# Kernel optimization log

Measured on AMD Instinct MI355X. Metric: run time of the kernel, lower is better.

The kernel has to match this reference:

```python
import jax, jax.numpy as jnp
import numpy as np

B, T, C, H = 2, 2048, 1024, 16
D = C // H  # head_dim = 64
CH = C // 2


def _ln(x, g, b, eps=1e-5):
    m = x.mean(-1, keepdims=True)
    v = ((x - m) ** 2).mean(-1, keepdims=True)
    return (x - m) / jnp.sqrt(v + eps) * g + b


def setup_inputs() -> dict:
    key = jax.random.key(0)
    ks = iter(jax.random.split(key, 32))
    w = lambda shp: jax.random.normal(next(ks), shp, dtype=jnp.float32) * 0.02
    inp = {
        'x': jax.random.normal(next(ks), (B, T, C), dtype=jnp.float32),
        'attention_mask': jnp.ones((B, T, T), dtype=jnp.int32),
        # importance_net: Linear(C,C/2), LN(C/2), GELU, Linear(C/2,1), Sigmoid
        'imp_w1': w((C, CH)), 'imp_b1': jnp.zeros((CH,)),
        'imp_g': jnp.ones((CH,)), 'imp_beta': jnp.zeros((CH,)),
        'imp_w2': w((CH, 1)), 'imp_b2': jnp.zeros((1,)),
        # reasoning_net: Linear(C,C), LN(C), GELU, Linear(C,C)
        'rsn_w1': w((C, C)), 'rsn_b1': jnp.zeros((C,)),
        'rsn_g': jnp.ones((C,)), 'rsn_beta': jnp.zeros((C,)),
        'rsn_w2': w((C, C)), 'rsn_b2': jnp.zeros((C,)),
        # attention projections
        'q_w': w((C, C)), 'q_b': jnp.zeros((C,)),
        'k_w': w((C, C)), 'k_b': jnp.zeros((C,)),
        'v_w': w((C, C)), 'v_b': jnp.zeros((C,)),
        'o_w': w((C, C)), 'o_b': jnp.zeros((C,)),
        # temp_net: Linear(C,C/2), LN(C/2), GELU, Linear(C/2,H)
        'tmp_w1': w((C, CH)), 'tmp_b1': jnp.zeros((CH,)),
        'tmp_g': jnp.ones((CH,)), 'tmp_beta': jnp.zeros((CH,)),
        'tmp_w2': w((CH, H)), 'tmp_b2': jnp.zeros((H,)),
        # output LayerNorm
        'norm_g': jnp.ones((C,)), 'norm_b': jnp.zeros((C,)),
    }
    return inp


def reference(x, attention_mask, imp_w1, imp_b1, imp_g, imp_beta, imp_w2, imp_b2,
              rsn_w1, rsn_b1, rsn_g, rsn_beta, rsn_w2, rsn_b2,
              q_w, q_b, k_w, k_b, v_w, v_b, o_w, o_b,
              tmp_w1, tmp_b1, tmp_g, tmp_beta, tmp_w2, tmp_b2,
              norm_g, norm_b):
    Bz, Tz, Cz = x.shape
    # importance gating: [B,T,1]
    h = jax.nn.gelu(_ln(x @ imp_w1 + imp_b1, imp_g, imp_beta), approximate=False)
    importance = jnp.maximum(jax.nn.sigmoid(h @ imp_w2 + imp_b2), 1e-6)
    xi = x * importance
    # reasoning net on gated input
    h = jax.nn.gelu(_ln(xi @ rsn_w1 + rsn_b1, rsn_g, rsn_beta), approximate=False)
    reasoned = h @ rsn_w2 + rsn_b2
    # projections
    q = (reasoned @ q_w + q_b).reshape(Bz, Tz, H, D).transpose(0, 2, 1, 3)
    k = (xi @ k_w + k_b).reshape(Bz, Tz, H, D).transpose(0, 2, 1, 3)
    v = (x @ v_w + v_b).reshape(Bz, Tz, H, D).transpose(0, 2, 1, 3)
    # per-(batch,head) temperature
    ht = jax.nn.gelu(_ln(reasoned.mean(axis=1) @ tmp_w1 + tmp_b1, tmp_g, tmp_beta), approximate=False)
    temp = jax.nn.softplus(ht @ tmp_w2 + tmp_b2) + 0.5  # [B,H]
    # attention with mask and learned temperature before softmax
    scale = 1.0 / jnp.sqrt(jnp.float32(D))
    attn = jnp.einsum('bhqd,bhkd->bhqk', q, k) * scale
    attn = jnp.where(attention_mask[:, None] == 0, -jnp.inf, attn)
    attn = attn * temp[:, :, None, None]
    attn = jax.nn.softmax(attn, axis=-1)
    # dropout is identity in eval mode
    out = jnp.einsum('bhqk,bhkd->bhqd', attn, v)
    out = out.transpose(0, 2, 1, 3).reshape(Bz, Tz, Cz)
    out = out @ o_w + o_b
    return _ln(x + out, norm_g, norm_b)
```

## Files before the change

### kernel.cpp

```cpp
#include <hip/hip_runtime.h>
#include <hip/hip_bf16.h>
#include <math.h>

#define BB 2
#define TT 2048
#define CC 1024
#define HH 16
#define DD 64
#define CHALF 512
#define NN (BB * TT)
#define LOG2E 1.44269504088896340736f

typedef __attribute__((ext_vector_type(8))) short short8;
typedef __attribute__((ext_vector_type(4))) short short4_t;
typedef __attribute__((ext_vector_type(4))) float f32x4;

__device__ __forceinline__ float gelu_exact(float x) {
    return 0.5f * x * (1.0f + erff(x * 0.70710678118654752f));
}

__device__ __forceinline__ short f2bf(float f) {
    __hip_bfloat16 h = __float2bfloat16(f);
    short s;
    __builtin_memcpy(&s, &h, 2);
    return s;
}

__device__ __forceinline__ float bf2f(short s) {
    __hip_bfloat16 h;
    __builtin_memcpy(&h, &s, 2);
    return __bfloat162float(h);
}

__device__ __forceinline__ short4_t pack_bf16x4(float a, float b, float c,
                                                float d) {
    short4_t s4;
    s4[0] = f2bf(a);
    s4[1] = f2bf(b);
    s4[2] = f2bf(c);
    s4[3] = f2bf(d);
    return s4;
}

__device__ __forceinline__ void async_copy16(const void* g, void* l) {
    __builtin_amdgcn_global_load_lds(
        (const __attribute__((address_space(1))) void*)g,
        (__attribute__((address_space(3))) void*)l, 16, 0, 0);
}

__global__ __launch_bounds__(256) void prep(
    const float* __restrict__ x, __hip_bfloat16* __restrict__ x_bf,
    const int* __restrict__ mask, int* __restrict__ flags,
    const float* w0, const float* w1, const float* w2, const float* w3,
    const float* w4, const float* w5, const float* w6,
    __hip_bfloat16* t0, __hip_bfloat16* t1, __hip_bfloat16* t2,
    __hip_bfloat16* t3, __hip_bfloat16* t4, __hip_bfloat16* t5,
    __hip_bfloat16* t6) {
    __shared__ float T[64][65];
    int blk = blockIdx.x;
    int tid = threadIdx.x;
    if (blk < 2048) {
        int i = (blk * 256 + tid) * 8;
        float4 a = *(const float4*)&x[i];
        float4 b = *(const float4*)&x[i + 4];
        __hip_bfloat16 o[8] = {
            __float2bfloat16(a.x), __float2bfloat16(a.y),
            __float2bfloat16(a.z), __float2bfloat16(a.w),
            __float2bfloat16(b.x), __float2bfloat16(b.y),
            __float2bfloat16(b.z), __float2bfloat16(b.w)};
        *(float4*)&x_bf[i] = *(float4*)o;
    } else if (blk < 4096) {
        int idx = blk - 2048;
        int kt = idx & 31, qt = (idx >> 5) & 31, b = idx >> 10;
        int* red = (int*)T;
        int r = tid >> 2;
        int c0 = (tid & 3) * 16;
        const int* base =
            mask + ((size_t)(b * TT + qt * 64 + r)) * TT + kt * 64 + c0;
        int all = 1;
#pragma unroll
        for (int i = 0; i < 4; ++i) {
            int4 m4 = *(const int4*)(base + i * 4);
            all &= (m4.x != 0) & (m4.y != 0) & (m4.z != 0) & (m4.w != 0);
        }
        red[tid] = all;
        __syncthreads();
#pragma unroll
        for (int o = 128; o > 0; o >>= 1) {
            if (tid < o) red[tid] &= red[tid + o];
            __syncthreads();
        }
        if (tid == 0) flags[(b * 32 + qt) * 32 + kt] = red[0];
    } else {
        int idx = blk - 4096;
        const float* W;
        __hip_bfloat16* Wt;
        int N, n0, k0;
        if (idx < 128) {
            W = w0; Wt = t0; N = 512;
            n0 = (idx & 7) * 64;
            k0 = (idx >> 3) * 64;
        } else {
            idx -= 128;
            int w = idx >> 8;
            int r = idx & 255;
            N = 1024;
            n0 = (r & 15) * 64;
            k0 = (r >> 4) * 64;
            switch (w) {
                case 0: W = w1; Wt = t1; break;
                case 1: W = w2; Wt = t2; break;
                case 2: W = w3; Wt = t3; break;
                case 3: W = w4; Wt = t4; break;
                case 4: W = w5; Wt = t5; break;
                default: W = w6; Wt = t6; break;
            }
        }
        int c = tid & 63, r4 = tid >> 6;
#pragma unroll
        for (int i = 0; i < 16; ++i) {
            int row = i * 4 + r4;
            T[row][c] = W[(size_t)(k0 + row) * N + n0 + c];
        }
        __syncthreads();
#pragma unroll
        for (int i = 0; i < 16; ++i) {
            int row = i * 4 + r4;
            Wt[(size_t)(n0 + row) * CC + k0 + c] = __float2bfloat16(T[c][row]);
        }
    }
}

template <bool BF16OUT>
__global__ __launch_bounds__(256) void gemm_mfma64(
    const short* __restrict__ A, const short* __restrict__ Wt,
    const float* __restrict__ bias, float* __restrict__ Cf,
    __hip_bfloat16* __restrict__ Cb, int M, int N, int K) {
    __shared__ short As0[64][32], As1[64][32];
    __shared__ short Bs0[128][32], Bs1[128][32];
    int tid = threadIdx.x;
    int wave = tid >> 6, lane = tid & 63;
    int m16 = lane & 15, quad = lane >> 4;
    int wm = wave >> 1, wn = wave & 1;
    int row0 = blockIdx.y * 64, col0 = blockIdx.x * 128;
    int lr = lane >> 2;
    int kof = (lane & 3) * 8;

    f32x4 acc[2][4];
#pragma unroll
    for (int i = 0; i < 2; ++i)
#pragma unroll
        for (int j = 0; j < 4; ++j) acc[i][j] = (f32x4){0.f, 0.f, 0.f, 0.f};

    for (int k0 = 0; k0 < K; k0 += 64) {
        const short* arow = A + (size_t)(row0 + wave * 16 + lr) * K + k0 + kof;
        async_copy16(arow, &As0[wave * 16][0]);
        async_copy16(arow + 32, &As1[wave * 16][0]);
#pragma unroll
        for (int j = 0; j < 2; ++j) {
            int rbase = wave * 32 + j * 16;
            const short* brow =
                Wt + (size_t)(col0 + rbase + lr) * K + k0 + kof;
            async_copy16(brow, &Bs0[rbase][0]);
            async_copy16(brow + 32, &Bs1[rbase][0]);
        }
        __syncthreads();
#pragma unroll
        for (int kc = 0; kc < 2; ++kc) {
            short8 af[2], bfr[4];
#pragma unroll
            for (int i = 0; i < 2; ++i)
                af[i] = kc ? *(const short8*)&As1[wm * 32 + i * 16 + m16][quad * 8]
                           : *(const short8*)&As0[wm * 32 + i * 16 + m16][quad * 8];
#pragma unroll
            for (int j = 0; j < 4; ++j)
                bfr[j] = kc ? *(const short8*)&Bs1[wn * 64 + j * 16 + m16][quad * 8]
                            : *(const short8*)&Bs0[wn * 64 + j * 16 + m16][quad * 8];
#pragma unroll
            for (int i = 0; i < 2; ++i)
#pragma unroll
                for (int j = 0; j < 4; ++j)
                    acc[i][j] = __builtin_amdgcn_mfma_f32_16x16x32_bf16(
                        af[i], bfr[j], acc[i][j], 0, 0, 0);
        }
        __syncthreads();
    }
#pragma unroll
    for (int i = 0; i < 2; ++i) {
#pragma unroll
        for (int j = 0; j < 4; ++j) {
            int col = col0 + wn * 64 + j * 16 + m16;
            float bv = bias[col];
#pragma unroll
            for (int rr = 0; rr < 4; ++rr) {
                int row = row0 + wm * 32 + i * 16 + quad * 4 + rr;
                float val = acc[i][j][rr] + bv;
                if (BF16OUT)
                    Cb[(size_t)row * N + col] = __float2bfloat16(val);
                else
                    Cf[(size_t)row * N + col] = val;
            }
        }
    }
}

__global__ __launch_bounds__(256) void gemm_qkv(
    const short* __restrict__ Aq, const short* __restrict__ Ak,
    const short* __restrict__ Av, const short* __restrict__ Wq,
    const short* __restrict__ Wk, const short* __restrict__ Wv,
    const float* __restrict__ bq, const float* __restrict__ bk,
    const float* __restrict__ bv, __hip_bfloat16* __restrict__ Cq,
    __hip_bfloat16* __restrict__ Ck, __hip_bfloat16* __restrict__ Cv,
    const float* __restrict__ tmp) {
    int z = blockIdx.z;
    const short* A = (z == 0) ? Aq : (z == 1) ? Ak : Av;
    const short* Wt = (z == 0) ? Wq : (z == 1) ? Wk : Wv;
    const float* bias = (z == 0) ? bq : (z == 1) ? bk : bv;

    __shared__ short As0[128][32], As1[128][32];
    __shared__ short Bs0[128][32], Bs1[128][32];
    int tid = threadIdx.x;
    int wave = tid >> 6, lane = tid & 63;
    int m16 = lane & 15, quad = lane >> 4;
    int wm = wave >> 1, wn = wave & 1;
    int row0 = blockIdx.y * 128, col0 = blockIdx.x * 128;
    int lr = lane >> 2;
    int kof = (lane & 3) * 8;

    float scale = 1.0f;
    if (z == 0)
        scale = tmp[(row0 >> 11) * HH + (col0 >> 6) + wn] * 0.125f * LOG2E;

    f32x4 acc[4][4];
#pragma unroll
    for (int i = 0; i < 4; ++i)
#pragma unroll
        for (int j = 0; j < 4; ++j) acc[i][j] = (f32x4){0.f, 0.f, 0.f, 0.f};

    for (int k0 = 0; k0 < CC; k0 += 64) {
#pragma unroll
        for (int j = 0; j < 2; ++j) {
            int rbase = wave * 32 + j * 16;
            const short* ar = A + (size_t)(row0 + rbase + lr) * CC + k0 + kof;
            async_copy16(ar, &As0[rbase][0]);
            async_copy16(ar + 32, &As1[rbase][0]);
            const short* br = Wt + (size_t)(col0 + rbase + lr) * CC + k0 + kof;
            async_copy16(br, &Bs0[rbase][0]);
            async_copy16(br + 32, &Bs1[rbase][0]);
        }
        __syncthreads();
#pragma unroll
        for (int kc = 0; kc < 2; ++kc) {
            short8 af[4], bfr[4];
#pragma unroll
            for (int i = 0; i < 4; ++i)
                af[i] = kc ? *(const short8*)&As1[wm * 64 + i * 16 + m16][quad * 8]
                           : *(const short8*)&As0[wm * 64 + i * 16 + m16][quad * 8];
#pragma unroll
            for (int j = 0; j < 4; ++j)
                bfr[j] = kc ? *(const short8*)&Bs1[wn * 64 + j * 16 + m16][quad * 8]
                            : *(const short8*)&Bs0[wn * 64 + j * 16 + m16][quad * 8];
#pragma unroll
            for (int i = 0; i < 4; ++i)
#pragma unroll
                for (int j = 0; j < 4; ++j)
                    acc[i][j] = __builtin_amdgcn_mfma_f32_16x16x32_bf16(
                        af[i], bfr[j], acc[i][j], 0, 0, 0);
        }
        __syncthreads();
    }
    if (z == 2) {
        int b = row0 >> 11;
        int t0r = (row0 & (TT - 1)) + wm * 64 + quad * 4;
#pragma unroll
        for (int i = 0; i < 4; ++i) {
#pragma unroll
            for (int j = 0; j < 4; ++j) {
                int col = col0 + wn * 64 + j * 16 + m16;
                int h = col >> 6, d = col & 63;
                float bv2 = bias[col];
                short4_t pk = pack_bf16x4(
                    acc[i][j][0] + bv2, acc[i][j][1] + bv2,
                    acc[i][j][2] + bv2, acc[i][j][3] + bv2);
                *(short4_t*)&Cv[(((size_t)(b * HH + h) * DD) + d) * TT + t0r +
                                i * 16] = pk;
            }
        }
    } else {
        __hip_bfloat16* C = (z == 0) ? Cq : Ck;
#pragma unroll
        for (int i = 0; i < 4; ++i) {
#pragma unroll
            for (int j = 0; j < 4; ++j) {
                int col = col0 + wn * 64 + j * 16 + m16;
                float bv2 = bias[col];
#pragma unroll
                for (int rr = 0; rr < 4; ++rr) {
                    int row = row0 + wm * 64 + i * 16 + quad * 4 + rr;
                    C[(size_t)row * CC + col] =
                        __float2bfloat16((acc[i][j][rr] + bv2) * scale);
                }
            }
        }
    }
}

__global__ __launch_bounds__(256) void imp_fused(
    const float* __restrict__ h1, const float* __restrict__ g,
    const float* __restrict__ beta, const float* __restrict__ w2,
    const float* __restrict__ b2, const float* __restrict__ x,
    __hip_bfloat16* __restrict__ xi) {
    int row = blockIdx.x;
    int tid = threadIdx.x;
    const float* hr = h1 + (size_t)row * CHALF;
    float v0 = hr[tid], v1 = hr[tid + 256];
    __shared__ float red[256];
    red[tid] = v0 + v1;
    __syncthreads();
#pragma unroll
    for (int o = 128; o > 0; o >>= 1) {
        if (tid < o) red[tid] += red[tid + o];
        __syncthreads();
    }
    float mean = red[0] * (1.0f / CHALF);
    __syncthreads();
    float d0 = v0 - mean, d1 = v1 - mean;
    red[tid] = d0 * d0 + d1 * d1;
    __syncthreads();
#pragma unroll
    for (int o = 128; o > 0; o >>= 1) {
        if (tid < o) red[tid] += red[tid + o];
        __syncthreads();
    }
    float inv = rsqrtf(red[0] * (1.0f / CHALF) + 1e-5f);
    __syncthreads();
    float ge0 = gelu_exact(d0 * inv * g[tid] + beta[tid]);
    float ge1 = gelu_exact(d1 * inv * g[tid + 256] + beta[tid + 256]);
    red[tid] = ge0 * w2[tid] + ge1 * w2[tid + 256];
    __syncthreads();
#pragma unroll
    for (int o = 128; o > 0; o >>= 1) {
        if (tid < o) red[tid] += red[tid + o];
        __syncthreads();
    }
    float z = red[0] + b2[0];
    float sg = 1.0f / (1.0f + expf(-z));
    float imp = fmaxf(sg, 1e-6f);
#pragma unroll
    for (int i = 0; i < 4; ++i) {
        int c = i * 256 + tid;
        xi[(size_t)row * CC + c] =
            __float2bfloat16(x[(size_t)row * CC + c] * imp);
    }
}

__global__ __launch_bounds__(256) void ln_gelu_bb(
    const __hip_bfloat16* __restrict__ Y, const float* __restrict__ g,
    const float* __restrict__ beta, __hip_bfloat16* __restrict__ O) {
    int row = blockIdx.x;
    int tid = threadIdx.x;
    int c0 = tid * 4;
    short4_t raw = *(const short4_t*)&Y[(size_t)row * CC + c0];
    float v[4];
    float s = 0.f;
#pragma unroll
    for (int i = 0; i < 4; ++i) {
        v[i] = bf2f(raw[i]);
        s += v[i];
    }
    __shared__ float red[256];
    red[tid] = s;
    __syncthreads();
#pragma unroll
    for (int o = 128; o > 0; o >>= 1) {
        if (tid < o) red[tid] += red[tid + o];
        __syncthreads();
    }
    float mean = red[0] * (1.0f / CC);
    __syncthreads();
    s = 0.f;
#pragma unroll
    for (int i = 0; i < 4; ++i) {
        float d = v[i] - mean;
        s += d * d;
    }
    red[tid] = s;
    __syncthreads();
#pragma unroll
    for (int o = 128; o > 0; o >>= 1) {
        if (tid < o) red[tid] += red[tid + o];
        __syncthreads();
    }
    float inv = rsqrtf(red[0] * (1.0f / CC) + 1e-5f);
    float4 gg = *(const float4*)&g[c0];
    float4 bb = *(const float4*)&beta[c0];
    short4_t ov = pack_bf16x4(
        gelu_exact((v[0] - mean) * inv * gg.x + bb.x),
        gelu_exact((v[1] - mean) * inv * gg.y + bb.y),
        gelu_exact((v[2] - mean) * inv * gg.z + bb.z),
        gelu_exact((v[3] - mean) * inv * gg.w + bb.w));
    *(short4_t*)&O[(size_t)row * CC + c0] = ov;
}

__global__ __launch_bounds__(256) void mean_part(
    const __hip_bfloat16* __restrict__ R, float* __restrict__ part) {
    int idx = blockIdx.x * 256 + threadIdx.x;
    int c = idx & (CC - 1);
    int chunk = (idx >> 10) & 15;
    int b = idx >> 14;
    const __hip_bfloat16* base = R + ((size_t)(b * TT + chunk * 128)) * CC + c;
    float s = 0.f;
    for (int t = 0; t < 128; ++t) s += __bfloat162float(base[(size_t)t * CC]);
    part[idx] = s;
}

__global__ __launch_bounds__(256) void temp_gemv1(
    const float* __restrict__ part, const float* __restrict__ w1,
    const float* __restrict__ b1, float* __restrict__ acc1) {
    __shared__ float rm_l[CC];
    __shared__ float red[256];
    int b = blockIdx.y;
    int c0 = blockIdx.x * 64;
    int tid = threadIdx.x;
    for (int cc = tid; cc < CC; cc += 256) {
        float s = 0.f;
#pragma unroll
        for (int ch = 0; ch < 16; ++ch)
            s += part[(size_t)(b * 16 + ch) * CC + cc];
        rm_l[cc] = s * (1.0f / TT);
    }
    __syncthreads();
    int col = c0 + (tid & 63);
    int kq = tid >> 6;
    float s = 0.f;
#pragma unroll 8
    for (int i = kq * 256; i < kq * 256 + 256; ++i)
        s = fmaf(rm_l[i], w1[(size_t)i * CHALF + col], s);
    red[tid] = s;
    __syncthreads();
    if (tid < 64) {
        float t = red[tid] + red[tid + 64] + red[tid + 128] + red[tid + 192];
        acc1[b * CHALF + tid + c0] = t + b1[col];
    }
}

__global__ __launch_bounds__(512) void temp_fin(
    const float* __restrict__ acc1, const float* __restrict__ g,
    const float* __restrict__ beta, const float* __restrict__ w2,
    const float* __restrict__ b2, float* __restrict__ temp) {
    __shared__ float red[512];
    __shared__ float wred[8][16];
    int b = blockIdx.x;
    int tid = threadIdx.x;
    int wave = tid >> 6, lane = tid & 63;
    float acc = acc1[b * CHALF + tid];
    red[tid] = acc;
    __syncthreads();
#pragma unroll
    for (int o = 256; o > 0; o >>= 1) {
        if (tid < o) red[tid] += red[tid + o];
        __syncthreads();
    }
    float mean = red[0] * (1.0f / CHALF);
    __syncthreads();
    float d = acc - mean;
    red[tid] = d * d;
    __syncthreads();
#pragma unroll
    for (int o = 256; o > 0; o >>= 1) {
        if (tid < o) red[tid] += red[tid + o];
        __syncthreads();
    }
    float inv = rsqrtf(red[0] * (1.0f / CHALF) + 1e-5f);
    float ht = gelu_exact((acc - mean) * inv * g[tid] + beta[tid]);
    float p[16];
#pragma unroll
    for (int j = 0; j < 16; ++j) p[j] = ht * w2[tid * HH + j];
#pragma unroll
    for (int off = 1; off < 64; off <<= 1)
#pragma unroll
        for (int j = 0; j < 16; ++j) p[j] += __shfl_xor(p[j], off, 64);
    if (lane == 0)
#pragma unroll
        for (int j = 0; j < 16; ++j) wred[wave][j] = p[j];
    __syncthreads();
    if (tid < HH) {
        float s = b2[tid];
#pragma unroll
        for (int w = 0; w < 8; ++w) s += wred[w][tid];
        float sp = fmaxf(s, 0.f) + log1pf(expf(-fabsf(s)));
        temp[b * HH + tid] = sp + 0.5f;
    }
}

__global__ __launch_bounds__(256) void flash_attn_mfma(
    const short* __restrict__ q, const short* __restrict__ k,
    const short* __restrict__ vt, const int* __restrict__ mask,
    const int* __restrict__ flags, __hip_bfloat16* __restrict__ out) {
    __shared__ short Ks[64][72];
    __shared__ short Vt[64][72];
    __shared__ short Ps[128][72];
    int tid = threadIdx.x;
    int wave = tid >> 6, lane = tid & 63;
    int m16 = lane & 15, quad = lane >> 4;
    int qt = blockIdx.x;
    int q0 = qt * 128;
    int bh = blockIdx.y;
    int b = bh >> 4, h = bh & 15;

    short8 qf[2][2];
#pragma unroll
    for (int qg = 0; qg < 2; ++qg) {
        const short* qrow = q + ((size_t)(b * TT + q0 + wave * 32 + qg * 16 + m16)) * CC +
                            h * DD + quad * 8;
        qf[qg][0] = *(const short8*)(qrow);
        qf[qg][1] = *(const short8*)(qrow + 32);
    }

    float m_run[2] = {-INFINITY, -INFINITY};
    float l_run[2] = {0.f, 0.f};
    f32x4 acc_o[2][4];
#pragma unroll
    for (int qg = 0; qg < 2; ++qg)
#pragma unroll
        for (int t = 0; t < 4; ++t) acc_o[qg][t] = (f32x4){0.f, 0.f, 0.f, 0.f};

    for (int kt = 0; kt < TT / 64; ++kt) {
        int kb = kt * 64;
#pragma unroll
        for (int i = 0; i < 2; ++i) {
            int idx = i * 256 + tid;
            int r = idx >> 3;
            int dc = (idx & 7) * 8;
            *(short8*)&Ks[r][dc] =
                *(const short8*)(k + ((size_t)(b * TT + kb + r)) * CC + h * DD + dc);
            *(short8*)&Vt[r][dc] =
                *(const short8*)(vt + ((size_t)bh * DD + r) * TT + kb + dc);
        }
        __syncthreads();

        short8 kf[4][2];
#pragma unroll
        for (int t = 0; t < 4; ++t) {
            kf[t][0] = *(const short8*)&Ks[t * 16 + m16][quad * 8];
            kf[t][1] = *(const short8*)&Ks[t * 16 + m16][32 + quad * 8];
        }
        int fl = flags[(b * 32 + 2 * qt + (wave >> 1)) * 32 + kt];

#pragma unroll
        for (int qg = 0; qg < 2; ++qg) {
            f32x4 sacc[4];
#pragma unroll
            for (int t = 0; t < 4; ++t) sacc[t] = (f32x4){0.f, 0.f, 0.f, 0.f};
#pragma unroll
            for (int t = 0; t < 4; ++t) {
                sacc[t] = __builtin_amdgcn_mfma_f32_16x16x32_bf16(kf[t][0], qf[qg][0], sacc[t], 0, 0, 0);
                sacc[t] = __builtin_amdgcn_mfma_f32_16x16x32_bf16(kf[t][1], qf[qg][1], sacc[t], 0, 0, 0);
            }
            float sv[4][4];
#pragma unroll
            for (int t = 0; t < 4; ++t)
#pragma unroll
                for (int r = 0; r < 4; ++r) sv[t][r] = sacc[t][r];
            if (fl == 0) {
                int qrow = q0 + wave * 32 + qg * 16 + m16;
#pragma unroll
                for (int t = 0; t < 4; ++t)
#pragma unroll
                    for (int r = 0; r < 4; ++r) {
                        int kg = kb + t * 16 + quad * 4 + r;
                        if (mask[((size_t)(b * TT + qrow)) * TT + kg] == 0)
                            sv[t][r] = -INFINITY;
                    }
            }
            float mx = sv[0][0];
#pragma unroll
            for (int t = 0; t < 4; ++t)
#pragma unroll
                for (int r = 0; r < 4; ++r) mx = fmaxf(mx, sv[t][r]);
            mx = fmaxf(mx, __shfl_xor(mx, 16, 64));
            mx = fmaxf(mx, __shfl_xor(mx, 32, 64));
            float mnew = fmaxf(m_run[qg], mx);
            if (__any(mnew > m_run[qg])) {
                float alpha = __builtin_amdgcn_exp2f(m_run[qg] - mnew);
                l_run[qg] *= alpha;
#pragma unroll
                for (int td = 0; td < 4; ++td)
#pragma unroll
                    for (int r = 0; r < 4; ++r) acc_o[qg][td][r] *= alpha;
            }
            m_run[qg] = mnew;
            int prow = wave * 32 + qg * 16 + m16;
            float psum = 0.f;
#pragma unroll
            for (int t = 0; t < 4; ++t) {
                short4_t pk;
#pragma unroll
                for (int r = 0; r < 4; ++r) {
                    float p = __builtin_amdgcn_exp2f(sv[t][r] - mnew);
                    psum += p;
                    pk[r] = f2bf(p);
                }
                *(short4_t*)&Ps[prow][t * 16 + quad * 4] = pk;
            }
            psum += __shfl_xor(psum, 16, 64);
            psum += __shfl_xor(psum, 32, 64);
            l_run[qg] += psum;
        }

#pragma unroll
        for (int kc = 0; kc < 2; ++kc) {
            short8 vf[4];
#pragma unroll
            for (int td = 0; td < 4; ++td)
                vf[td] = *(const short8*)&Vt[td * 16 + m16][kc * 32 + quad * 8];
#pragma unroll
            for (int qg = 0; qg < 2; ++qg) {
                short8 pf = *(const short8*)&Ps[wave * 32 + qg * 16 + m16][kc * 32 + quad * 8];
#pragma unroll
                for (int td = 0; td < 4; ++td)
                    acc_o[qg][td] = __builtin_amdgcn_mfma_f32_16x16x32_bf16(
                        vf[td], pf, acc_o[qg][td], 0, 0, 0);
            }
        }
        __syncthreads();
    }

#pragma unroll
    for (int qg = 0; qg < 2; ++qg) {
        float inv = 1.0f / l_run[qg];
        int row = b * TT + q0 + wave * 32 + qg * 16 + m16;
#pragma unroll
        for (int td = 0; td < 4; ++td) {
            short4_t pk = pack_bf16x4(
                acc_o[qg][td][0] * inv, acc_o[qg][td][1] * inv,
                acc_o[qg][td][2] * inv, acc_o[qg][td][3] * inv);
            *(short4_t*)&out[(size_t)row * CC + h * DD + td * 16 + quad * 4] = pk;
        }
    }
}

__global__ __launch_bounds__(256) void final_ln_b(
    const float* __restrict__ x, const __hip_bfloat16* __restrict__ p,
    const float* __restrict__ g, const float* __restrict__ beta,
    float* __restrict__ out) {
    int row = blockIdx.x;
    int tid = threadIdx.x;
    int c0 = tid * 4;
    float4 xv = *(const float4*)&x[(size_t)row * CC + c0];
    short4_t pv = *(const short4_t*)&p[(size_t)row * CC + c0];
    float v[4] = {xv.x + bf2f(pv[0]), xv.y + bf2f(pv[1]),
                  xv.z + bf2f(pv[2]), xv.w + bf2f(pv[3])};
    float s = v[0] + v[1] + v[2] + v[3];
    __shared__ float red[256];
    red[tid] = s;
    __syncthreads();
#pragma unroll
    for (int o = 128; o > 0; o >>= 1) {
        if (tid < o) red[tid] += red[tid + o];
        __syncthreads();
    }
    float mean = red[0] * (1.0f / CC);
    __syncthreads();
    s = 0.f;
#pragma unroll
    for (int i = 0; i < 4; ++i) {
        float d = v[i] - mean;
        s += d * d;
    }
    red[tid] = s;
    __syncthreads();
#pragma unroll
    for (int o = 128; o > 0; o >>= 1) {
        if (tid < o) red[tid] += red[tid + o];
        __syncthreads();
    }
    float inv = rsqrtf(red[0] * (1.0f / CC) + 1e-5f);
    float4 gg = *(const float4*)&g[c0];
    float4 bb = *(const float4*)&beta[c0];
    float4 ov = {(v[0] - mean) * inv * gg.x + bb.x,
                 (v[1] - mean) * inv * gg.y + bb.y,
                 (v[2] - mean) * inv * gg.z + bb.z,
                 (v[3] - mean) * inv * gg.w + bb.w};
    *(float4*)&out[(size_t)row * CC + c0] = ov;
}

extern "C" void kernel_launch(void* const* d_in, const int* in_sizes, int n_in,
                              void* d_out, int out_size, void* d_ws,
                              size_t ws_size, hipStream_t stream) {
    const float* x        = (const float*)d_in[0];
    const int*   mask     = (const int*)d_in[1];
    const float* imp_w1   = (const float*)d_in[2];
    const float* imp_b1   = (const float*)d_in[3];
    const float* imp_g    = (const float*)d_in[4];
    const float* imp_beta = (const float*)d_in[5];
    const float* imp_w2   = (const float*)d_in[6];
    const float* imp_b2   = (const float*)d_in[7];
    const float* rsn_w1   = (const float*)d_in[8];
    const float* rsn_b1   = (const float*)d_in[9];
    const float* rsn_g    = (const float*)d_in[10];
    const float* rsn_beta = (const float*)d_in[11];
    const float* rsn_w2   = (const float*)d_in[12];
    const float* rsn_b2   = (const float*)d_in[13];
    const float* q_w      = (const float*)d_in[14];
    const float* q_b      = (const float*)d_in[15];
    const float* k_w      = (const float*)d_in[16];
    const float* k_b      = (const float*)d_in[17];
    const float* v_w      = (const float*)d_in[18];
    const float* v_b      = (const float*)d_in[19];
    const float* o_w      = (const float*)d_in[20];
    const float* o_b      = (const float*)d_in[21];
    const float* tmp_w1   = (const float*)d_in[22];
    const float* tmp_b1   = (const float*)d_in[23];
    const float* tmp_g    = (const float*)d_in[24];
    const float* tmp_beta = (const float*)d_in[25];
    const float* tmp_w2   = (const float*)d_in[26];
    const float* tmp_b2   = (const float*)d_in[27];
    const float* norm_g   = (const float*)d_in[28];
    const float* norm_b   = (const float*)d_in[29];
    float* out = (float*)d_out;
    float* ws  = (float*)d_ws;

    float* h1  = ws;
    __hip_bfloat16* g1b   = (__hip_bfloat16*)(ws + 2097152);
    __hip_bfloat16* x_bf  = (__hip_bfloat16*)(ws + 6291456);
    __hip_bfloat16* xi_bf = (__hip_bfloat16*)(ws + 8388608);
    __hip_bfloat16* h2b   = (__hip_bfloat16*)(ws + 10485760);
    __hip_bfloat16* rs_bf = (__hip_bfloat16*)(ws + 12582912);
    __hip_bfloat16* qb    = (__hip_bfloat16*)(ws + 14680064);
    __hip_bfloat16* kb    = (__hip_bfloat16*)(ws + 16777216);
    __hip_bfloat16* vtb   = (__hip_bfloat16*)(ws + 20971520);
    __hip_bfloat16* imp_w1t = (__hip_bfloat16*)(ws + 23068672);
    __hip_bfloat16* rsn_w1t = (__hip_bfloat16*)(ws + 23330816);
    __hip_bfloat16* rsn_w2t = (__hip_bfloat16*)(ws + 23855104);
    __hip_bfloat16* q_wt    = (__hip_bfloat16*)(ws + 24379392);
    __hip_bfloat16* k_wt    = (__hip_bfloat16*)(ws + 24903680);
    __hip_bfloat16* v_wt    = (__hip_bfloat16*)(ws + 25427968);
    __hip_bfloat16* o_wt    = (__hip_bfloat16*)(ws + 25952256);
    float* tmp  = ws + 26478592;
    float* part = ws + 26479104;
    int*   flg  = (int*)(ws + 26511872);
    float* acc1 = ws + 26513920;

    dim3 blk(256);
    prep<<<5760, blk, 0, stream>>>(
        x, x_bf, mask, flg,
        imp_w1, rsn_w1, rsn_w2, q_w, k_w, v_w, o_w,
        imp_w1t, rsn_w1t, rsn_w2t, q_wt, k_wt, v_wt, o_wt);

    gemm_mfma64<false><<<dim3(CHALF / 128, NN / 64), blk, 0, stream>>>(
        (const short*)x_bf, (const short*)imp_w1t, imp_b1, h1, nullptr, NN, CHALF, CC);
    imp_fused<<<NN, blk, 0, stream>>>(h1, imp_g, imp_beta, imp_w2, imp_b2, x, xi_bf);
    gemm_mfma64<true><<<dim3(CC / 128, NN / 64), blk, 0, stream>>>(
        (const short*)xi_bf, (const short*)rsn_w1t, rsn_b1, nullptr, g1b, NN, CC, CC);
    ln_gelu_bb<<<NN, blk, 0, stream>>>(g1b, rsn_g, rsn_beta, h2b);
    gemm_mfma64<true><<<dim3(CC / 128, NN / 64), blk, 0, stream>>>(
        (const short*)h2b, (const short*)rsn_w2t, rsn_b2, nullptr, rs_bf, NN, CC, CC);
    mean_part<<<128, blk, 0, stream>>>(rs_bf, part);
    temp_gemv1<<<dim3(CHALF / 64, BB), blk, 0, stream>>>(part, tmp_w1, tmp_b1, acc1);
    temp_fin<<<BB, dim3(512), 0, stream>>>(acc1, tmp_g, tmp_beta, tmp_w2, tmp_b2, tmp);
    gemm_qkv<<<dim3(CC / 128, NN / 128, 3), blk, 0, stream>>>(
        (const short*)rs_bf, (const short*)xi_bf, (const short*)x_bf,
        (const short*)q_wt, (const short*)k_wt, (const short*)v_wt,
        q_b, k_b, v_b, qb, kb, vtb, tmp);
    flash_attn_mfma<<<dim3(TT / 128, BB * HH), blk, 0, stream>>>(
        (const short*)qb, (const short*)kb, (const short*)vtb, mask, flg, rs_bf);
    gemm_mfma64<true><<<dim3(CC / 128, NN / 64), blk, 0, stream>>>(
        (const short*)rs_bf, (const short*)o_wt, o_b, nullptr, g1b, NN, CC, CC);
    final_ln_b<<<NN, blk, 0, stream>>>(x, g1b, norm_g, norm_b, out);
}
```

Baseline: 412.7 us.

## Split flash attention over the key dimension and merge the halves in a combine kernel

```diff
diff --git a/kernel.cpp b/kernel.cpp
--- a/kernel.cpp
+++ b/kernel.cpp
@@ -496,7 +496,8 @@
 __global__ __launch_bounds__(256) void flash_attn_mfma(
     const short* __restrict__ q, const short* __restrict__ k,
     const short* __restrict__ vt, const int* __restrict__ mask,
-    const int* __restrict__ flags, __hip_bfloat16* __restrict__ out) {
+    const int* __restrict__ flags, __hip_bfloat16* __restrict__ po,
+    float* __restrict__ ml) {
     __shared__ short Ks[64][72];
     __shared__ short Vt[64][72];
     __shared__ short Ps[128][72];
@@ -507,6 +508,7 @@
     int q0 = qt * 128;
     int bh = blockIdx.y;
     int b = bh >> 4, h = bh & 15;
+    int zi = blockIdx.z;
 
     short8 qf[2][2];
 #pragma unroll
@@ -525,7 +527,7 @@
 #pragma unroll
         for (int t = 0; t < 4; ++t) acc_o[qg][t] = (f32x4){0.f, 0.f, 0.f, 0.f};
 
-    for (int kt = 0; kt < TT / 64; ++kt) {
+    for (int kt = zi * 16; kt < zi * 16 + 16; ++kt) {
         int kb = kt * 64;
 #pragma unroll
         for (int i = 0; i < 2; ++i) {
@@ -628,16 +630,42 @@
 
 #pragma unroll
     for (int qg = 0; qg < 2; ++qg) {
-        float inv = 1.0f / l_run[qg];
-        int row = b * TT + q0 + wave * 32 + qg * 16 + m16;
+        int qrow = q0 + wave * 32 + qg * 16 + m16;
+        size_t base = ((size_t)zi * (BB * HH) + bh) * TT + qrow;
+        if (quad == 0) {
+            float2 v2 = make_float2(m_run[qg], l_run[qg]);
+            *(float2*)&ml[base * 2] = v2;
+        }
 #pragma unroll
         for (int td = 0; td < 4; ++td) {
-            short4_t pk = pack_bf16x4(
-                acc_o[qg][td][0] * inv, acc_o[qg][td][1] * inv,
-                acc_o[qg][td][2] * inv, acc_o[qg][td][3] * inv);
-            *(short4_t*)&out[(size_t)row * CC + h * DD + td * 16 + quad * 4] = pk;
-        }
-    }
+            short4_t pk = pack_bf16x4(acc_o[qg][td][0], acc_o[qg][td][1],
+                                      acc_o[qg][td][2], acc_o[qg][td][3]);
+            *(short4_t*)&po[base * DD + td * 16 + quad * 4] = pk;
+        }
+    }
+}
+
+__global__ __launch_bounds__(256) void flash_combine(
+    const __hip_bfloat16* __restrict__ po, const float* __restrict__ ml,
+    __hip_bfloat16* __restrict__ out) {
+    int i = blockIdx.x * 256 + threadIdx.x;
+    int d0 = (i & 15) * 4;
+    int qg = i >> 4;
+    float2 ml0 = *(const float2*)&ml[(size_t)qg * 2];
+    float2 ml1 = *(const float2*)&ml[(size_t)(65536 + qg) * 2];
+    float m = fmaxf(ml0.x, ml1.x);
+    float w0 = __builtin_amdgcn_exp2f(ml0.x - m);
+    float w1 = __builtin_amdgcn_exp2f(ml1.x - m);
+    float inv = 1.0f / (ml0.y * w0 + ml1.y * w1);
+    short4_t o0 = *(const short4_t*)&po[(size_t)qg * DD + d0];
+    short4_t o1 = *(const short4_t*)&po[(size_t)(65536 + qg) * DD + d0];
+    int bh = qg >> 11, qrow = qg & (TT - 1);
+    int b = bh >> 4, h = bh & 15;
+    short4_t ov;
+#pragma unroll
+    for (int r = 0; r < 4; ++r)
+        ov[r] = f2bf((bf2f(o0[r]) * w0 + bf2f(o1[r]) * w1) * inv);
+    *(short4_t*)&out[((size_t)(b * TT + qrow)) * CC + h * DD + d0] = ov;
 }
 
 __global__ __launch_bounds__(256) void final_ln_b(
@@ -723,6 +751,7 @@
 
     float* h1  = ws;
     __hip_bfloat16* g1b   = (__hip_bfloat16*)(ws + 2097152);
+    __hip_bfloat16* po    = (__hip_bfloat16*)ws;
     __hip_bfloat16* x_bf  = (__hip_bfloat16*)(ws + 6291456);
     __hip_bfloat16* xi_bf = (__hip_bfloat16*)(ws + 8388608);
     __hip_bfloat16* h2b   = (__hip_bfloat16*)(ws + 10485760);
@@ -741,6 +770,7 @@
     float* part = ws + 26479104;
     int*   flg  = (int*)(ws + 26511872);
     float* acc1 = ws + 26513920;
+    float* ml   = ws + 26514944;
 
     dim3 blk(256);
     prep<<<5760, blk, 0, stream>>>(
@@ -763,8 +793,10 @@
         (const short*)rs_bf, (const short*)xi_bf, (const short*)x_bf,
         (const short*)q_wt, (const short*)k_wt, (const short*)v_wt,
         q_b, k_b, v_b, qb, kb, vtb, tmp);
-    flash_attn_mfma<<<dim3(TT / 128, BB * HH), blk, 0, stream>>>(
-        (const short*)qb, (const short*)kb, (const short*)vtb, mask, flg, rs_bf);
+    flash_attn_mfma<<<dim3(TT / 128, BB * HH, 2), blk, 0, stream>>>(
+        (const short*)qb, (const short*)kb, (const short*)vtb, mask, flg,
+        po, ml);
+    flash_combine<<<4096, blk, 0, stream>>>(po, ml, rs_bf);
     gemm_mfma64<true><<<dim3(CC / 128, NN / 64), blk, 0, stream>>>(
         (const short*)rs_bf, (const short*)o_wt, o_b, nullptr, g1b, NN, CC, CC);
     final_ln_b<<<NN, blk, 0, stream>>>(x, g1b, norm_g, norm_b, out);
```

After: 423.3 us. 2.6% more time.

## Fold reasoning_net second linear into Q projection weights

Applied to the files above, without the earlier changes.

```diff
diff --git a/kernel.cpp b/kernel.cpp
--- a/kernel.cpp
+++ b/kernel.cpp
@@ -93,9 +93,21 @@
         if (tid == 0) flags[(b * 32 + qt) * 32 + kt] = red[0];
     } else {
         int idx = blk - 4096;
+        if (idx >= 1408) {
+            int i = (idx - 1408) * 2048 + tid * 8;
+            float4 a = *(const float4*)&w2[i];
+            float4 b = *(const float4*)&w2[i + 4];
+            __hip_bfloat16 o[8] = {
+                __float2bfloat16(a.x), __float2bfloat16(a.y),
+                __float2bfloat16(a.z), __float2bfloat16(a.w),
+                __float2bfloat16(b.x), __float2bfloat16(b.y),
+                __float2bfloat16(b.z), __float2bfloat16(b.w)};
+            *(float4*)&t2[i] = *(float4*)o;
+            return;
+        }
         const float* W;
         __hip_bfloat16* Wt;
-        int N, n0, k0;
+        int N = 1024, n0, k0;
         if (idx < 128) {
             W = w0; Wt = t0; N = 512;
             n0 = (idx & 7) * 64;
@@ -104,15 +116,13 @@
             idx -= 128;
             int w = idx >> 8;
             int r = idx & 255;
-            N = 1024;
             n0 = (r & 15) * 64;
             k0 = (r >> 4) * 64;
             switch (w) {
                 case 0: W = w1; Wt = t1; break;
-                case 1: W = w2; Wt = t2; break;
-                case 2: W = w3; Wt = t3; break;
-                case 3: W = w4; Wt = t4; break;
-                case 4: W = w5; Wt = t5; break;
+                case 1: W = w3; Wt = t3; break;
+                case 2: W = w4; Wt = t4; break;
+                case 3: W = w5; Wt = t5; break;
                 default: W = w6; Wt = t6; break;
             }
         }
@@ -305,6 +315,25 @@
     }
 }
 
+__global__ __launch_bounds__(256) void bias_qc_kernel(
+    const short* __restrict__ q_wt, const float* __restrict__ rsn_b2,
+    const float* __restrict__ q_b, float* __restrict__ bias_qc) {
+    int j = blockIdx.x * 4 + (threadIdx.x >> 6);
+    int lane = threadIdx.x & 63;
+    const short* row = q_wt + (size_t)j * CC + lane * 16;
+    short8 a0 = *(const short8*)row;
+    short8 a1 = *(const short8*)(row + 8);
+    float s = 0.f;
+#pragma unroll
+    for (int u = 0; u < 8; ++u) s = fmaf(bf2f(a0[u]), rsn_b2[lane * 16 + u], s);
+#pragma unroll
+    for (int u = 0; u < 8; ++u)
+        s = fmaf(bf2f(a1[u]), rsn_b2[lane * 16 + 8 + u], s);
+#pragma unroll
+    for (int off = 1; off < 64; off <<= 1) s += __shfl_xor(s, off, 64);
+    if (lane == 0) bias_qc[j] = s + q_b[j];
+}
+
 __global__ __launch_bounds__(256) void imp_fused(
     const float* __restrict__ h1, const float* __restrict__ g,
     const float* __restrict__ beta, const float* __restrict__ w2,
@@ -414,21 +443,45 @@
     part[idx] = s;
 }
 
+__global__ __launch_bounds__(256) void rm_proj(
+    const float* __restrict__ part, const short* __restrict__ rsn_w2r,
+    const float* __restrict__ rsn_b2, float* __restrict__ rm) {
+    __shared__ float mh[CC];
+    __shared__ float red[256];
+    int b = blockIdx.y;
+    int c0 = blockIdx.x * 64;
+    int tid = threadIdx.x;
+    for (int cc = tid; cc < CC; cc += 256) {
+        float s = 0.f;
+#pragma unroll
+        for (int ch = 0; ch < 16; ++ch)
+            s += part[(size_t)(b * 16 + ch) * CC + cc];
+        mh[cc] = s * (1.0f / TT);
+    }
+    __syncthreads();
+    int col = c0 + (tid & 63);
+    int kq = tid >> 6;
+    float s = 0.f;
+#pragma unroll 8
+    for (int i = kq * 256; i < kq * 256 + 256; ++i)
+        s = fmaf(mh[i], bf2f(rsn_w2r[(size_t)i * CC + col]), s);
+    red[tid] = s;
+    __syncthreads();
+    if (tid < 64) {
+        float t = red[tid] + red[tid + 64] + red[tid + 128] + red[tid + 192];
+        rm[b * CC + c0 + tid] = t + rsn_b2[c0 + tid];
+    }
+}
+
 __global__ __launch_bounds__(256) void temp_gemv1(
-    const float* __restrict__ part, const float* __restrict__ w1,
+    const float* __restrict__ rm, const float* __restrict__ w1,
     const float* __restrict__ b1, float* __restrict__ acc1) {
     __shared__ float rm_l[CC];
     __shared__ float red[256];
     int b = blockIdx.y;
     int c0 = blockIdx.x * 64;
     int tid = threadIdx.x;
-    for (int cc = tid; cc < CC; cc += 256) {
-        float s = 0.f;
-#pragma unroll
-        for (int ch = 0; ch < 16; ++ch)
-            s += part[(size_t)(b * 16 + ch) * CC + cc];
-        rm_l[cc] = s * (1.0f / TT);
-    }
+    for (int cc = tid; cc < CC; cc += 256) rm_l[cc] = rm[b * CC + cc];
     __syncthreads();
     int col = c0 + (tid & 63);
     int kq = tid >> 6;
@@ -727,12 +780,13 @@
     __hip_bfloat16* xi_bf = (__hip_bfloat16*)(ws + 8388608);
     __hip_bfloat16* h2b   = (__hip_bfloat16*)(ws + 10485760);
     __hip_bfloat16* rs_bf = (__hip_bfloat16*)(ws + 12582912);
+    __hip_bfloat16* w_qct = rs_bf;
     __hip_bfloat16* qb    = (__hip_bfloat16*)(ws + 14680064);
+    __hip_bfloat16* rsn_w2r = qb;
     __hip_bfloat16* kb    = (__hip_bfloat16*)(ws + 16777216);
     __hip_bfloat16* vtb   = (__hip_bfloat16*)(ws + 20971520);
     __hip_bfloat16* imp_w1t = (__hip_bfloat16*)(ws + 23068672);
     __hip_bfloat16* rsn_w1t = (__hip_bfloat16*)(ws + 23330816);
-    __hip_bfloat16* rsn_w2t = (__hip_bfloat16*)(ws + 23855104);
     __hip_bfloat16* q_wt    = (__hip_bfloat16*)(ws + 24379392);
     __hip_bfloat16* k_wt    = (__hip_bfloat16*)(ws + 24903680);
     __hip_bfloat16* v_wt    = (__hip_bfloat16*)(ws + 25427968);
@@ -741,28 +795,36 @@
     float* part = ws + 26479104;
     int*   flg  = (int*)(ws + 26511872);
     float* acc1 = ws + 26513920;
+    float* zeros   = ws + 26514944;
+    float* bias_qc = ws + 26515968;
+    float* rm      = ws + 26516992;
 
     dim3 blk(256);
-    prep<<<5760, blk, 0, stream>>>(
+    hipMemsetAsync(zeros, 0, 1024 * sizeof(float), stream);
+    prep<<<6016, blk, 0, stream>>>(
         x, x_bf, mask, flg,
         imp_w1, rsn_w1, rsn_w2, q_w, k_w, v_w, o_w,
-        imp_w1t, rsn_w1t, rsn_w2t, q_wt, k_wt, v_wt, o_wt);
-
+        imp_w1t, rsn_w1t, rsn_w2r, q_wt, k_wt, v_wt, o_wt);
+    gemm_mfma64<true><<<dim3(CC / 128, 1024 / 64), blk, 0, stream>>>(
+        (const short*)q_wt, (const short*)rsn_w2r, zeros, nullptr, w_qct,
+        1024, CC, CC);
+    bias_qc_kernel<<<256, blk, 0, stream>>>((const short*)q_wt, rsn_b2, q_b,
+                                            bias_qc);
     gemm_mfma64<false><<<dim3(CHALF / 128, NN / 64), blk, 0, stream>>>(
         (const short*)x_bf, (const short*)imp_w1t, imp_b1, h1, nullptr, NN, CHALF, CC);
     imp_fused<<<NN, blk, 0, stream>>>(h1, imp_g, imp_beta, imp_w2, imp_b2, x, xi_bf);
     gemm_mfma64<true><<<dim3(CC / 128, NN / 64), blk, 0, stream>>>(
         (const short*)xi_bf, (const short*)rsn_w1t, rsn_b1, nullptr, g1b, NN, CC, CC);
     ln_gelu_bb<<<NN, blk, 0, stream>>>(g1b, rsn_g, rsn_beta, h2b);
-    gemm_mfma64<true><<<dim3(CC / 128, NN / 64), blk, 0, stream>>>(
-        (const short*)h2b, (const short*)rsn_w2t, rsn_b2, nullptr, rs_bf, NN, CC, CC);
-    mean_part<<<128, blk, 0, stream>>>(rs_bf, part);
-    temp_gemv1<<<dim3(CHALF / 64, BB), blk, 0, stream>>>(part, tmp_w1, tmp_b1, acc1);
+    mean_part<<<128, blk, 0, stream>>>(h2b, part);
+    rm_proj<<<dim3(CC / 64, BB), blk, 0, stream>>>(part, (const short*)rsn_w2r,
+                                                   rsn_b2, rm);
+    temp_gemv1<<<dim3(CHALF / 64, BB), blk, 0, stream>>>(rm, tmp_w1, tmp_b1, acc1);
     temp_fin<<<BB, dim3(512), 0, stream>>>(acc1, tmp_g, tmp_beta, tmp_w2, tmp_b2, tmp);
     gemm_qkv<<<dim3(CC / 128, NN / 128, 3), blk, 0, stream>>>(
-        (const short*)rs_bf, (const short*)xi_bf, (const short*)x_bf,
-        (const short*)q_wt, (const short*)k_wt, (const short*)v_wt,
-        q_b, k_b, v_b, qb, kb, vtb, tmp);
+        (const short*)h2b, (const short*)xi_bf, (const short*)x_bf,
+        (const short*)w_qct, (const short*)k_wt, (const short*)v_wt,
+        bias_qc, k_b, v_b, qb, kb, vtb, tmp);
     flash_attn_mfma<<<dim3(TT / 128, BB * HH), blk, 0, stream>>>(
         (const short*)qb, (const short*)kb, (const short*)vtb, mask, flg, rs_bf);
     gemm_mfma64<true><<<dim3(CC / 128, NN / 64), blk, 0, stream>>>(
```

Result: slower. 438.4 us (+6.2%).

## Double-buffer K/V tiles in flash attention with register prefetch

Applied to the files above, without the earlier changes.

```diff
diff --git a/kernel.cpp b/kernel.cpp
--- a/kernel.cpp
+++ b/kernel.cpp
@@ -497,8 +497,8 @@
     const short* __restrict__ q, const short* __restrict__ k,
     const short* __restrict__ vt, const int* __restrict__ mask,
     const int* __restrict__ flags, __hip_bfloat16* __restrict__ out) {
-    __shared__ short Ks[64][72];
-    __shared__ short Vt[64][72];
+    __shared__ short Ks[2][64][72];
+    __shared__ short Vt[2][64][72];
     __shared__ short Ps[128][72];
     int tid = threadIdx.x;
     int wave = tid >> 6, lane = tid & 63;
@@ -508,6 +508,14 @@
     int bh = blockIdx.y;
     int b = bh >> 4, h = bh & 15;
 
+    int sr[2], sdc[2];
+#pragma unroll
+    for (int i = 0; i < 2; ++i) {
+        int idx = i * 256 + tid;
+        sr[i] = idx >> 3;
+        sdc[i] = (idx & 7) * 8;
+    }
+
     short8 qf[2][2];
 #pragma unroll
     for (int qg = 0; qg < 2; ++qg) {
@@ -525,25 +533,36 @@
 #pragma unroll
         for (int t = 0; t < 4; ++t) acc_o[qg][t] = (f32x4){0.f, 0.f, 0.f, 0.f};
 
+#pragma unroll
+    for (int i = 0; i < 2; ++i) {
+        *(short8*)&Ks[0][sr[i]][sdc[i]] =
+            *(const short8*)(k + ((size_t)(b * TT + sr[i])) * CC + h * DD + sdc[i]);
+        *(short8*)&Vt[0][sr[i]][sdc[i]] =
+            *(const short8*)(vt + ((size_t)bh * DD + sr[i]) * TT + sdc[i]);
+    }
+    __syncthreads();
+
     for (int kt = 0; kt < TT / 64; ++kt) {
+        int cur = kt & 1, nxt = cur ^ 1;
+        short8 kreg[2], vreg[2];
+        bool have_next = (kt + 1 < TT / 64);
+        if (have_next) {
+            int kb2 = (kt + 1) * 64;
+#pragma unroll
+            for (int i = 0; i < 2; ++i) {
+                kreg[i] = *(const short8*)(k + ((size_t)(b * TT + kb2 + sr[i])) * CC +
+                                           h * DD + sdc[i]);
+                vreg[i] = *(const short8*)(vt + ((size_t)bh * DD + sr[i]) * TT +
+                                           kb2 + sdc[i]);
+            }
+        }
+
         int kb = kt * 64;
-#pragma unroll
-        for (int i = 0; i < 2; ++i) {
-            int idx = i * 256 + tid;
-            int r = idx >> 3;
-            int dc = (idx & 7) * 8;
-            *(short8*)&Ks[r][dc] =
-                *(const short8*)(k + ((size_t)(b * TT + kb + r)) * CC + h * DD + dc);
-            *(short8*)&Vt[r][dc] =
-                *(const short8*)(vt + ((size_t)bh * DD + r) * TT + kb + dc);
-        }
-        __syncthreads();
-
         short8 kf[4][2];
 #pragma unroll
         for (int t = 0; t < 4; ++t) {
-            kf[t][0] = *(const short8*)&Ks[t * 16 + m16][quad * 8];
-            kf[t][1] = *(const short8*)&Ks[t * 16 + m16][32 + quad * 8];
+            kf[t][0] = *(const short8*)&Ks[cur][t * 16 + m16][quad * 8];
+            kf[t][1] = *(const short8*)&Ks[cur][t * 16 + m16][32 + quad * 8];
         }
         int fl = flags[(b * 32 + 2 * qt + (wave >> 1)) * 32 + kt];
 
@@ -613,7 +632,7 @@
             short8 vf[4];
 #pragma unroll
             for (int td = 0; td < 4; ++td)
-                vf[td] = *(const short8*)&Vt[td * 16 + m16][kc * 32 + quad * 8];
+                vf[td] = *(const short8*)&Vt[cur][td * 16 + m16][kc * 32 + quad * 8];
 #pragma unroll
             for (int qg = 0; qg < 2; ++qg) {
                 short8 pf = *(const short8*)&Ps[wave * 32 + qg * 16 + m16][kc * 32 + quad * 8];
@@ -621,6 +640,14 @@
                 for (int td = 0; td < 4; ++td)
                     acc_o[qg][td] = __builtin_amdgcn_mfma_f32_16x16x32_bf16(
                         vf[td], pf, acc_o[qg][td], 0, 0, 0);
+            }
+        }
+
+        if (have_next) {
+#pragma unroll
+            for (int i = 0; i < 2; ++i) {
+                *(short8*)&Ks[nxt][sr[i]][sdc[i]] = kreg[i];
+                *(short8*)&Vt[nxt][sr[i]][sdc[i]] = vreg[i];
             }
         }
         __syncthreads();
```

Result: no change. 412.2 us (-0.1%).
